# Optimization experiments

Measured on AMD Instinct MI355X. Metric: run time of the kernel, lower is better.

## Reference

```python
import jax, jax.numpy as jnp
import numpy as np

B, S, D, N, L, V = 4, 2048, 512, 16, 4, 256
EPS = 1e-5


def layernorm(x, g, b):
    m = x.mean(-1, keepdims=True)
    v = ((x - m) ** 2).mean(-1, keepdims=True)
    return (x - m) * jax.lax.rsqrt(v + EPS) * g + b


def ssm_layer(x, logA, Wd, bd, WB, bB, WC, bC, WDp, bDp, g, be):
    # x: (B,S,D)
    h = layernorm(x, g, be)
    delta = jax.nn.softplus(h @ Wd + bd)          # (B,S,D)
    Bi = h @ WB + bB                              # (B,S,N)
    Ci = h @ WC + bC                              # (B,S,N)
    A = -jnp.exp(logA)                            # (D,N)

    def step(state, inp):
        d_t, b_t, c_t, h_t = inp                  # (B,D),(B,N),(B,N),(B,D)
        dA = jnp.exp(d_t[:, :, None] * A)         # (B,D,N)
        state = dA * state + (d_t * h_t)[:, :, None] * b_t[:, None, :]
        y_t = jnp.einsum('bdn,bn->bd', state, c_t)
        return state, y_t

    xs = (jnp.moveaxis(delta, 1, 0), jnp.moveaxis(Bi, 1, 0),
          jnp.moveaxis(Ci, 1, 0), jnp.moveaxis(h, 1, 0))
    init = jnp.zeros((x.shape[0], x.shape[2], logA.shape[-1]), x.dtype)
    _, ys = jax.lax.scan(step, init, xs)
    y = jnp.moveaxis(ys, 0, 1)                    # (B,S,D)
    return x + y + h @ WDp + bDp


def setup_inputs() -> dict:
    key = jax.random.key(0)
    ks = jax.random.split(key, 12)
    s = 0.02
    byte_ids = jax.random.randint(ks[0], (B, S), 0, 256)
    emb_byte = jax.random.normal(ks[1], (V, D), jnp.float32) * s
    emb_pos = jax.random.normal(ks[2], (S, D), jnp.float32) * s
    logA = jnp.tile(jnp.log(jnp.linspace(1.0, N, N, dtype=jnp.float32)), (L, D, 1))
    Wd = jax.random.normal(ks[3], (L, D, D), jnp.float32) * s
    bd = jnp.zeros((L, D), jnp.float32)
    WB = jax.random.normal(ks[4], (L, D, N), jnp.float32) * s
    bB = jnp.zeros((L, N), jnp.float32)
    WC = jax.random.normal(ks[5], (L, D, N), jnp.float32) * s
    bC = jnp.zeros((L, N), jnp.float32)
    WDp = jax.random.normal(ks[6], (L, D, D), jnp.float32) * s
    bDp = jnp.zeros((L, D), jnp.float32)
    gamma = jnp.ones((L, D), jnp.float32)
    beta = jnp.zeros((L, D), jnp.float32)
    Wh = jax.random.normal(ks[7], (D, V), jnp.float32) * s
    bh = jnp.zeros((V,), jnp.float32)
    return {'byte_ids': byte_ids, 'emb_byte': emb_byte, 'emb_pos': emb_pos,
            'logA': logA, 'Wd': Wd, 'bd': bd, 'WB': WB, 'bB': bB,
            'WC': WC, 'bC': bC, 'WDp': WDp, 'bDp': bDp,
            'gamma': gamma, 'beta': beta, 'Wh': Wh, 'bh': bh}


def reference(byte_ids, emb_byte, emb_pos, logA, Wd, bd, WB, bB, WC, bC,
              WDp, bDp, gamma, beta, Wh, bh):
    S_ = byte_ids.shape[1]
    h = emb_byte[byte_ids] + emb_pos[:S_]
    for l in range(Wd.shape[0]):
        h = ssm_layer(h, logA[l], Wd[l], bd[l], WB[l], bB[l], WC[l], bC[l],
                      WDp[l], bDp[l], gamma[l], beta[l])
    return h @ Wh + bh                            # (B,S,256) logits
```

## Files before the change

### kernel.cpp

```cpp
#include <hip/hip_runtime.h>
#include <math.h>

#define BB 4
#define SS 2048
#define DD 512
#define NN 16
#define LL 4
#define VV 256
#define CC 64
#define TT (SS / CC)
#define EPSL 1e-5f
#define MM (BB * SS)
#define KI 16
#define LPAD 528

typedef __bf16 bf16;
typedef __attribute__((ext_vector_type(8))) __bf16 bf16x8;
typedef __attribute__((ext_vector_type(4))) __bf16 bf16x4;
typedef __attribute__((ext_vector_type(4))) float f32x4;


#define GLD_LDS(g, l) \
    __builtin_amdgcn_global_load_lds((__attribute__((address_space(1))) void*)(void*)(g), \
                                     (__attribute__((address_space(3))) void*)(l), 16, 0, 0)

__device__ __forceinline__ void ln_row_write(float4 v0, float4 v1, int lane, size_t row,
                                             const float* __restrict__ gamma,
                                             const float* __restrict__ beta,
                                             float* HN, bf16* HNb) {
    float s = v0.x + v0.y + v0.z + v0.w + v1.x + v1.y + v1.z + v1.w;
    float q = v0.x * v0.x + v0.y * v0.y + v0.z * v0.z + v0.w * v0.w +
              v1.x * v1.x + v1.y * v1.y + v1.z * v1.z + v1.w * v1.w;
#pragma unroll
    for (int o = 1; o < 64; o <<= 1) {
        s += __shfl_xor(s, o);
        q += __shfl_xor(q, o);
    }
    float m = s * (1.0f / DD);
    float var = q * (1.0f / DD) - m * m;
    float rs = rsqrtf(var + EPSL);
    float4 g0 = *(const float4*)(gamma + lane * 4);
    float4 g1 = *(const float4*)(gamma + 256 + lane * 4);
    float4 b0 = *(const float4*)(beta + lane * 4);
    float4 b1 = *(const float4*)(beta + 256 + lane * 4);
    float4 o0, o1;
    o0.x = (v0.x - m) * rs * g0.x + b0.x;
    o0.y = (v0.y - m) * rs * g0.y + b0.y;
    o0.z = (v0.z - m) * rs * g0.z + b0.z;
    o0.w = (v0.w - m) * rs * g0.w + b0.w;
    o1.x = (v1.x - m) * rs * g1.x + b1.x;
    o1.y = (v1.y - m) * rs * g1.y + b1.y;
    o1.z = (v1.z - m) * rs * g1.z + b1.z;
    o1.w = (v1.w - m) * rs * g1.w + b1.w;
    float* hr = HN + row * DD;
    *(float4*)(hr + lane * 4) = o0;
    *(float4*)(hr + 256 + lane * 4) = o1;
    size_t pb = (size_t)(row >> 4) * 8192 + (size_t)(lane >> 3) * 512 +
                (size_t)((lane & 7) >> 1) * 128 + (row & 15) * 8 + (lane & 1) * 4;
    bf16x4 p0 = {(bf16)o0.x, (bf16)o0.y, (bf16)o0.z, (bf16)o0.w};
    bf16x4 p1 = {(bf16)o1.x, (bf16)o1.y, (bf16)o1.z, (bf16)o1.w};
    *(bf16x4*)(HNb + pb) = p0;
    *(bf16x4*)(HNb + pb + 8 * 512) = p1;
}

__global__ void embed_ln(const int* __restrict__ ids,
                         const float* __restrict__ eb,
                         const float* __restrict__ ep,
                         const float* __restrict__ gamma,
                         const float* __restrict__ beta,
                         float* __restrict__ X, float* HN, bf16* HNb) {
    int wave = threadIdx.x >> 6;
    int lane = threadIdx.x & 63;
    size_t row = blockIdx.x * 4 + wave;
    int s = (int)(row & (SS - 1));
    int id = ids[row];
    const float* ebr = eb + (size_t)id * DD;
    const float* epr = ep + (size_t)s * DD;
    float4 e0 = *(const float4*)(ebr + lane * 4);
    float4 e1 = *(const float4*)(ebr + 256 + lane * 4);
    float4 p0 = *(const float4*)(epr + lane * 4);
    float4 p1 = *(const float4*)(epr + 256 + lane * 4);
    float4 v0 = {e0.x + p0.x, e0.y + p0.y, e0.z + p0.z, e0.w + p0.w};
    float4 v1 = {e1.x + p1.x, e1.y + p1.y, e1.z + p1.z, e1.w + p1.w};
    *(float4*)(X + row * DD + lane * 4) = v0;
    *(float4*)(X + row * DD + 256 + lane * 4) = v1;
    ln_row_write(v0, v1, lane, row, gamma, beta, HN, HNb);
}

__global__ __launch_bounds__(256) void convert_weights(const float* __restrict__ Wd,
                                                       const float* __restrict__ WDp,
                                                       const float* __restrict__ Wh,
                                                       bf16* __restrict__ WtP) {
    __shared__ float slab[512 * 17];
    int blk = blockIdx.x;
    const float* src;
    int nsrc, col0;
    bf16* dst;
    if (blk < 256) {
        int l = blk >> 6, tile = blk & 63;
        src = (tile < 32) ? (Wd + (size_t)l * DD * DD) : (WDp + (size_t)l * DD * DD);
        col0 = (tile & 31) * 16;
        nsrc = DD;
        dst = WtP + ((size_t)l * 64 + tile) * 8192;
    } else {
        int tile = blk - 256;
        src = Wh;
        col0 = tile * 16;
        nsrc = VV;
        dst = WtP + (size_t)(256 + tile) * 8192;
    }
    int tid = threadIdx.x;
    int kr = tid >> 2, cq = tid & 3;
#pragma unroll
    for (int i = 0; i < 8; i++) {
        int k = i * 64 + kr;
        float4 v = *(const float4*)(src + (size_t)k * nsrc + col0 + cq * 4);
        slab[k * 17 + cq * 4 + 0] = v.x;
        slab[k * 17 + cq * 4 + 1] = v.y;
        slab[k * 17 + cq * 4 + 2] = v.z;
        slab[k * 17 + cq * 4 + 3] = v.w;
    }
    __syncthreads();
#pragma unroll
    for (int it = 0; it < 4; it++) {
        int c = it * 256 + tid;
        int ki = c >> 6, fq = (c >> 4) & 3, fm = c & 15;
        int k0 = ki * 32 + fq * 8;
        bf16x8 v;
#pragma unroll
        for (int e = 0; e < 8; e++) v[e] = (bf16)slab[(k0 + e) * 17 + fm];
        *(bf16x8*)(dst + (size_t)c * 8) = v;
    }
}

template <int MODE, int NT>
__global__ __launch_bounds__(256, 8) void gemm_pack(const bf16* __restrict__ Ap,
                                                    const bf16* __restrict__ Bp,
                                                    const float* __restrict__ bias,
                                                    const float* __restrict__ bias2,
                                                    const float* __restrict__ Xres,
                                                    float* __restrict__ O1,
                                                    float* __restrict__ O2, int Nout) {
    __shared__ bf16 As[4 * 512];
    __shared__ bf16 Bs[4 * 512];
    const int tid = threadIdx.x, wave = tid >> 6, lane = tid & 63;
    const int lin = blockIdx.x;
    const int xcd = lin & 7, i4 = lin >> 3;
    const int ms = xcd * 16 + (i4 & 15);
    const int nb = i4 >> 4;

    const bf16* gA = Ap + ((size_t)ms * 4 + wave) * 8192 + lane * 8;
    const bf16* gB = Bp + ((size_t)nb * 4 + wave) * 8192 + lane * 8;
    bf16* lA = As + wave * 512;
    bf16* lB = Bs + wave * 512;

    const int fa0 = (wave >> 1) * 2, fb0 = (wave & 1) * 2;

    f32x4 acc[2][2];
#pragma unroll
    for (int i = 0; i < 2; i++)
#pragma unroll
        for (int j = 0; j < 2; j++) acc[i][j] = (f32x4){0.f, 0.f, 0.f, 0.f};

    for (int ki = 0; ki < KI; ki++) {
        GLD_LDS(gA + ki * 512, lA);
        GLD_LDS(gB + ki * 512, lB);
        __syncthreads();
        bf16x8 af[2], bfr[2];
#pragma unroll
        for (int i = 0; i < 2; i++) af[i] = *(const bf16x8*)(As + (fa0 + i) * 512 + lane * 8);
#pragma unroll
        for (int j = 0; j < 2; j++) bfr[j] = *(const bf16x8*)(Bs + (fb0 + j) * 512 + lane * 8);
#pragma unroll
        for (int i = 0; i < 2; i++)
#pragma unroll
            for (int j = 0; j < 2; j++)
                acc[i][j] = __builtin_amdgcn_mfma_f32_16x16x32_bf16(af[i], bfr[j], acc[i][j], 0, 0, 0);
        __syncthreads();
    }

    const int fm = lane & 15, fq = lane >> 4;
#pragma unroll
    for (int i = 0; i < 2; i++) {
#pragma unroll
        for (int j = 0; j < 2; j++) {
            int col = (nb * 4 + fb0 + j) * 16 + fm;
#pragma unroll
            for (int r = 0; r < 4; r++) {
                int row = (ms * 4 + fa0 + i) * 16 + fq * 4 + r;
                float v = acc[i][j][r];
                if (MODE == 0) {
                    O1[(size_t)row * Nout + col] = v + bias[col];
                } else {
                    if (col < DD) {
                        v += bias[col];
                        v = fmaxf(v, 0.0f) + log1pf(__expf(-fabsf(v)));
                        O1[(size_t)row * DD + col] = v;
                    } else {
                        int c = col - DD;
                        O2[(size_t)row * DD + c] = v + bias2[c] + Xres[(size_t)row * DD + c];
                    }
                }
            }
        }
    }
}

__global__ void gemmBC(const float* __restrict__ HN,
                       const float* __restrict__ WB, const float* __restrict__ bB,
                       const float* __restrict__ WC, const float* __restrict__ bC,
                       float* __restrict__ BI, float* __restrict__ CI) {
    int tid = threadIdx.x;
    int col = tid & 15;
    int row = blockIdx.x * 16 + (tid >> 4);
    const float* ar = HN + (size_t)row * DD;
    float accB = 0.0f, accC = 0.0f;
#pragma unroll 8
    for (int k = 0; k < DD; k++) {
        float a = ar[k];
        accB = fmaf(a, WB[k * NN + col], accB);
        accC = fmaf(a, WC[k * NN + col], accC);
    }
    BI[(size_t)row * NN + col] = accB + bB[col];
    CI[(size_t)row * NN + col] = accC + bC[col];
}

__global__ __launch_bounds__(512) void scan1(const float* __restrict__ DEL,
                                             const float* __restrict__ HN,
                                             const float* __restrict__ BI,
                                             const float* __restrict__ logA,
                                             float* __restrict__ P,
                                             float* __restrict__ LSt) {
    int b = blockIdx.x / CC, c = blockIdx.x % CC;
    int d = threadIdx.x;
    float Ar[NN], prod[NN], st[NN];
#pragma unroll
    for (int n = 0; n < NN; n++) {
        Ar[n] = -__expf(logA[d * NN + n]);
        prod[n] = 1.0f;
        st[n] = 0.0f;
    }
    size_t row0 = (size_t)b * SS + c * TT;
    for (int tt = 0; tt < TT; tt++) {
        size_t base = row0 + tt;
        float dl = DEL[base * DD + d];
        float du = dl * HN[base * DD + d];
        const float* bi = BI + base * NN;
#pragma unroll
        for (int n = 0; n < NN; n++) {
            float a = __expf(dl * Ar[n]);
            prod[n] *= a;
            st[n] = fmaf(a, st[n], du * bi[n]);
        }
    }
    size_t o = (((size_t)b * DD + d) * CC + c) * NN;
#pragma unroll
    for (int n = 0; n < NN; n++) {
        P[o + n] = prod[n];
        LSt[o + n] = st[n];
    }
}

__global__ void scan2(const float* __restrict__ P, float* __restrict__ LS) {
    int tid = blockIdx.x * 256 + threadIdx.x;
    int n = tid & (NN - 1);
    int d = (tid / NN) & (DD - 1);
    int b = tid / (NN * DD);
    size_t base = ((size_t)b * DD + d) * CC;
    float s = 0.0f;
    for (int c = 0; c < CC; c++) {
        size_t o = base * NN + (size_t)c * NN + n;
        float p = P[o];
        float ls = LS[o];
        LS[o] = s;
        s = fmaf(p, s, ls);
    }
}

template <int LAST>
__global__ __launch_bounds__(512) void scan3ln(const float* __restrict__ DEL,
                                               float* HN,
                                               const float* __restrict__ BI,
                                               const float* __restrict__ CI,
                                               const float* __restrict__ logA,
                                               const float* __restrict__ SIN,
                                               const float* __restrict__ D2,
                                               const float* __restrict__ gamma,
                                               const float* __restrict__ beta,
                                               float* __restrict__ X,
                                               bf16* HNb) {
    __shared__ float xvs[32 * LPAD];
    int b = blockIdx.x / CC, c = blockIdx.x % CC;
    int d = threadIdx.x;
    float Ar[NN], st[NN];
    size_t o = (((size_t)b * DD + d) * CC + c) * NN;
#pragma unroll
    for (int n = 0; n < NN; n++) {
        Ar[n] = -__expf(logA[d * NN + n]);
        st[n] = SIN[o + n];
    }
    size_t row0 = (size_t)b * SS + c * TT;
    for (int tt = 0; tt < TT; tt++) {
        size_t base = row0 + tt;
        float dl = DEL[base * DD + d];
        float du = dl * HN[base * DD + d];
        const float* bi = BI + base * NN;
        const float* ci = CI + base * NN;
        float y = 0.0f;
#pragma unroll
        for (int n = 0; n < NN; n++) {
            float a = __expf(dl * Ar[n]);
            st[n] = fmaf(a, st[n], du * bi[n]);
            y = fmaf(st[n], ci[n], y);
        }
        float xv = D2[base * DD + d] + y;
        xvs[tt * LPAD + d] = xv;
        if (!LAST) X[base * DD + d] = xv;
    }
    __syncthreads();
    int wv = d >> 6, lane = d & 63;
#pragma unroll
    for (int r = 0; r < 4; r++) {
        int tt = wv * 4 + r;
        size_t row = row0 + tt;
        const float* xr = xvs + tt * LPAD;
        float4 v0 = *(const float4*)(xr + lane * 4);
        float4 v1 = *(const float4*)(xr + 256 + lane * 4);
        if (LAST) {
            size_t pb = (size_t)(row >> 4) * 8192 + (size_t)(lane >> 3) * 512 +
                        (size_t)((lane & 7) >> 1) * 128 + (row & 15) * 8 + (lane & 1) * 4;
            bf16x4 p0 = {(bf16)v0.x, (bf16)v0.y, (bf16)v0.z, (bf16)v0.w};
            bf16x4 p1 = {(bf16)v1.x, (bf16)v1.y, (bf16)v1.z, (bf16)v1.w};
            *(bf16x4*)(HNb + pb) = p0;
            *(bf16x4*)(HNb + pb + 8 * 512) = p1;
        } else {
            ln_row_write(v0, v1, lane, row, gamma, beta, HN, HNb);
        }
    }
}

extern "C" void kernel_launch(void* const* d_in, const int* in_sizes, int n_in,
                              void* d_out, int out_size, void* d_ws, size_t ws_size,
                              hipStream_t stream) {
    const int* ids = (const int*)d_in[0];
    const float* eb = (const float*)d_in[1];
    const float* ep = (const float*)d_in[2];
    const float* logA = (const float*)d_in[3];
    const float* Wd = (const float*)d_in[4];
    const float* bd = (const float*)d_in[5];
    const float* WB = (const float*)d_in[6];
    const float* bB = (const float*)d_in[7];
    const float* WC = (const float*)d_in[8];
    const float* bC = (const float*)d_in[9];
    const float* WDp = (const float*)d_in[10];
    const float* bDp = (const float*)d_in[11];
    const float* gamma = (const float*)d_in[12];
    const float* beta = (const float*)d_in[13];
    const float* Wh = (const float*)d_in[14];
    const float* bh = (const float*)d_in[15];
    float* out = (float*)d_out;

    size_t E = (size_t)MM * DD;
    size_t EN = (size_t)MM * NN;
    size_t EC = (size_t)BB * DD * CC * NN;
    float* X = (float*)d_ws;
    float* HN = X + E;
    float* DEL = HN + E;
    float* D2 = DEL + E;
    float* BIc = D2 + E;
    float* CIc = BIc + EN;
    float* P = CIc + EN;
    float* LS = P + EC;
    bf16* HNb = (bf16*)(LS + EC);
    bf16* WtP = HNb + E;

    embed_ln<<<MM / 4, 256, 0, stream>>>(ids, eb, ep, gamma, beta, X, HN, HNb);
    convert_weights<<<272, 256, 0, stream>>>(Wd, WDp, Wh, WtP);
    for (int l = 0; l < LL; l++) {
        const float* lA = logA + (size_t)l * DD * NN;
        gemm_pack<1, 16><<<2048, 256, 0, stream>>>(
            HNb, WtP + (size_t)l * 524288, bd + l * DD, bDp + l * DD, X, DEL, D2, 1024);
        gemmBC<<<MM / 16, 256, 0, stream>>>(HN, WB + (size_t)l * DD * NN, bB + l * NN,
                                            WC + (size_t)l * DD * NN, bC + l * NN, BIc, CIc);
        scan1<<<BB * CC, 512, 0, stream>>>(DEL, HN, BIc, lA, P, LS);
        scan2<<<(BB * DD * NN) / 256, 256, 0, stream>>>(P, LS);
        if (l < LL - 1) {
            scan3ln<0><<<BB * CC, 512, 0, stream>>>(DEL, HN, BIc, CIc, lA, LS, D2,
                                                    gamma + (l + 1) * DD, beta + (l + 1) * DD,
                                                    X, HNb);
        } else {
            scan3ln<1><<<BB * CC, 512, 0, stream>>>(DEL, HN, BIc, CIc, lA, LS, D2,
                                                    nullptr, nullptr, X, HNb);
        }
    }
    gemm_pack<0, 4><<<512, 256, 0, stream>>>(
        HNb, WtP + (size_t)2097152, bh, nullptr, nullptr, out, nullptr, VV);
}
```

Baseline: 546.7 us.

## Fuse B/C projection and three-pass chunked scan into one cooperative kernel

Replaces the gemmBC, scan1, scan2 and scan3ln launches with a single cooperative kernel that uses grid.sync between phases. Each block computes its chunk's B/C projections into shared memory and keeps delta and delta*h in registers across the first and third passes instead of re-reading them from global memory. The layernorm is now done with wave shuffles and no longer stages the chunk through a large shared buffer. This removes launch overhead and intermediate BI/CI traffic, at the cost of higher register pressure (arrays of 32 elements per thread), two grid-wide barriers, and a middle scan pass that runs on only 64 blocks.

```diff
diff --git a/kernel.cpp b/kernel.cpp
--- a/kernel.cpp
+++ b/kernel.cpp
@@ -1,4 +1,5 @@
 #include <hip/hip_runtime.h>
+#include <hip/hip_cooperative_groups.h>
 #include <math.h>
 
 #define BB 4
@@ -12,7 +13,8 @@
 #define EPSL 1e-5f
 #define MM (BB * SS)
 #define KI 16
-#define LPAD 528
+
+namespace cg = cooperative_groups;
 
 typedef __bf16 bf16;
 typedef __attribute__((ext_vector_type(8))) __bf16 bf16x8;
@@ -206,136 +208,142 @@
     }
 }
 
-__global__ void gemmBC(const float* __restrict__ HN,
-                       const float* __restrict__ WB, const float* __restrict__ bB,
-                       const float* __restrict__ WC, const float* __restrict__ bC,
-                       float* __restrict__ BI, float* __restrict__ CI) {
-    int tid = threadIdx.x;
-    int col = tid & 15;
-    int row = blockIdx.x * 16 + (tid >> 4);
-    const float* ar = HN + (size_t)row * DD;
-    float accB = 0.0f, accC = 0.0f;
+template <int LAST>
+__global__ __launch_bounds__(512, 2) void scan_coop(
+        const float* __restrict__ DEL, float* HN,
+        const float* __restrict__ WB, const float* __restrict__ bB,
+        const float* __restrict__ WC, const float* __restrict__ bC,
+        const float* __restrict__ logA, const float* __restrict__ D2,
+        const float* __restrict__ gamma, const float* __restrict__ beta,
+        float* __restrict__ X, bf16* __restrict__ HNb,
+        float* __restrict__ P, float* __restrict__ LS) {
+    cg::grid_group grid = cg::this_grid();
+    __shared__ float bis[TT * NN];
+    __shared__ float cis[TT * NN];
+    __shared__ float wred[2][8][TT];
+    __shared__ float rstat[TT * 2];
+
+    const int lin = blockIdx.x;
+    const int b = lin / CC, c = lin % CC;
+    const int tid = threadIdx.x;
+    const size_t row0 = (size_t)b * SS + c * TT;
+
+    {
+        int row = tid >> 4, col = tid & 15;
+        const float* hr = HN + (row0 + row) * DD;
+        float aB = 0.0f, aC = 0.0f;
 #pragma unroll 8
-    for (int k = 0; k < DD; k++) {
-        float a = ar[k];
-        accB = fmaf(a, WB[k * NN + col], accB);
-        accC = fmaf(a, WC[k * NN + col], accC);
-    }
-    BI[(size_t)row * NN + col] = accB + bB[col];
-    CI[(size_t)row * NN + col] = accC + bC[col];
-}
-
-__global__ __launch_bounds__(512) void scan1(const float* __restrict__ DEL,
-                                             const float* __restrict__ HN,
-                                             const float* __restrict__ BI,
-                                             const float* __restrict__ logA,
-                                             float* __restrict__ P,
-                                             float* __restrict__ LSt) {
-    int b = blockIdx.x / CC, c = blockIdx.x % CC;
-    int d = threadIdx.x;
-    float Ar[NN], prod[NN], st[NN];
+        for (int k = 0; k < DD; k++) {
+            float h = hr[k];
+            aB = fmaf(h, WB[k * NN + col], aB);
+            aC = fmaf(h, WC[k * NN + col], aC);
+        }
+        bis[row * NN + col] = aB + bB[col];
+        cis[row * NN + col] = aC + bC[col];
+    }
+    __syncthreads();
+
+    const int d = tid;
+    float Ar[NN], st[NN], prod[NN], dl[TT], du[TT];
 #pragma unroll
     for (int n = 0; n < NN; n++) {
         Ar[n] = -__expf(logA[d * NN + n]);
         prod[n] = 1.0f;
         st[n] = 0.0f;
     }
-    size_t row0 = (size_t)b * SS + c * TT;
+#pragma unroll
     for (int tt = 0; tt < TT; tt++) {
         size_t base = row0 + tt;
-        float dl = DEL[base * DD + d];
-        float du = dl * HN[base * DD + d];
-        const float* bi = BI + base * NN;
+        dl[tt] = DEL[base * DD + d];
+        du[tt] = dl[tt] * HN[base * DD + d];
 #pragma unroll
         for (int n = 0; n < NN; n++) {
-            float a = __expf(dl * Ar[n]);
+            float a = __expf(dl[tt] * Ar[n]);
             prod[n] *= a;
-            st[n] = fmaf(a, st[n], du * bi[n]);
-        }
-    }
-    size_t o = (((size_t)b * DD + d) * CC + c) * NN;
+            st[n] = fmaf(a, st[n], du[tt] * bis[tt * NN + n]);
+        }
+    }
+    const size_t o = (((size_t)b * DD + d) * CC + c) * NN;
 #pragma unroll
     for (int n = 0; n < NN; n++) {
         P[o + n] = prod[n];
-        LSt[o + n] = st[n];
-    }
-}
-
-__global__ void scan2(const float* __restrict__ P, float* __restrict__ LS) {
-    int tid = blockIdx.x * 256 + threadIdx.x;
-    int n = tid & (NN - 1);
-    int d = (tid / NN) & (DD - 1);
-    int b = tid / (NN * DD);
-    size_t base = ((size_t)b * DD + d) * CC;
-    float s = 0.0f;
-    for (int c = 0; c < CC; c++) {
-        size_t o = base * NN + (size_t)c * NN + n;
-        float p = P[o];
-        float ls = LS[o];
-        LS[o] = s;
-        s = fmaf(p, s, ls);
-    }
-}
-
-template <int LAST>
-__global__ __launch_bounds__(512) void scan3ln(const float* __restrict__ DEL,
-                                               float* HN,
-                                               const float* __restrict__ BI,
-                                               const float* __restrict__ CI,
-                                               const float* __restrict__ logA,
-                                               const float* __restrict__ SIN,
-                                               const float* __restrict__ D2,
-                                               const float* __restrict__ gamma,
-                                               const float* __restrict__ beta,
-                                               float* __restrict__ X,
-                                               bf16* HNb) {
-    __shared__ float xvs[32 * LPAD];
-    int b = blockIdx.x / CC, c = blockIdx.x % CC;
-    int d = threadIdx.x;
-    float Ar[NN], st[NN];
-    size_t o = (((size_t)b * DD + d) * CC + c) * NN;
-#pragma unroll
-    for (int n = 0; n < NN; n++) {
-        Ar[n] = -__expf(logA[d * NN + n]);
-        st[n] = SIN[o + n];
-    }
-    size_t row0 = (size_t)b * SS + c * TT;
+        LS[o + n] = st[n];
+    }
+    grid.sync();
+
+    if (lin < 64) {
+        int g = lin * 512 + tid;
+        int n2 = g & (NN - 1);
+        int d2 = (g >> 4) & (DD - 1);
+        int b2 = g >> 13;
+        size_t base2 = ((size_t)b2 * DD + d2) * CC;
+        float s = 0.0f;
+        for (int c2 = 0; c2 < CC; c2++) {
+            size_t oo = (base2 + c2) * NN + n2;
+            float p = P[oo];
+            float ls = LS[oo];
+            LS[oo] = s;
+            s = fmaf(p, s, ls);
+        }
+    }
+    grid.sync();
+
+    float xv[TT];
+#pragma unroll
+    for (int n = 0; n < NN; n++) st[n] = LS[o + n];
+#pragma unroll
     for (int tt = 0; tt < TT; tt++) {
         size_t base = row0 + tt;
-        float dl = DEL[base * DD + d];
-        float du = dl * HN[base * DD + d];
-        const float* bi = BI + base * NN;
-        const float* ci = CI + base * NN;
         float y = 0.0f;
 #pragma unroll
         for (int n = 0; n < NN; n++) {
-            float a = __expf(dl * Ar[n]);
-            st[n] = fmaf(a, st[n], du * bi[n]);
-            y = fmaf(st[n], ci[n], y);
-        }
-        float xv = D2[base * DD + d] + y;
-        xvs[tt * LPAD + d] = xv;
-        if (!LAST) X[base * DD + d] = xv;
-    }
-    __syncthreads();
-    int wv = d >> 6, lane = d & 63;
-#pragma unroll
-    for (int r = 0; r < 4; r++) {
-        int tt = wv * 4 + r;
+            float a = __expf(dl[tt] * Ar[n]);
+            st[n] = fmaf(a, st[n], du[tt] * bis[tt * NN + n]);
+            y = fmaf(st[n], cis[tt * NN + n], y);
+        }
+        xv[tt] = D2[base * DD + d] + y;
+        if (!LAST) X[base * DD + d] = xv[tt];
+    }
+
+    const int wv = tid >> 6, lane = tid & 63;
+    if (!LAST) {
+#pragma unroll
+        for (int tt = 0; tt < TT; tt++) {
+            float s1 = xv[tt], s2 = xv[tt] * xv[tt];
+#pragma unroll
+            for (int ofs = 1; ofs < 64; ofs <<= 1) {
+                s1 += __shfl_xor(s1, ofs);
+                s2 += __shfl_xor(s2, ofs);
+            }
+            if (lane == 0) { wred[0][wv][tt] = s1; wred[1][wv][tt] = s2; }
+        }
+        __syncthreads();
+        if (tid < TT) {
+            float s1 = 0.0f, s2 = 0.0f;
+#pragma unroll
+            for (int w = 0; w < 8; w++) { s1 += wred[0][w][tid]; s2 += wred[1][w][tid]; }
+            float m = s1 * (1.0f / DD);
+            float var = s2 * (1.0f / DD) - m * m;
+            rstat[tid * 2] = m;
+            rstat[tid * 2 + 1] = rsqrtf(var + EPSL);
+        }
+        __syncthreads();
+    }
+
+    float gd = 1.0f, bd_ = 0.0f;
+    if (!LAST) { gd = gamma[d]; bd_ = beta[d]; }
+    const int ki2 = d >> 5, fq2 = (d >> 3) & 3, e2 = d & 7;
+#pragma unroll
+    for (int tt = 0; tt < TT; tt++) {
         size_t row = row0 + tt;
-        const float* xr = xvs + tt * LPAD;
-        float4 v0 = *(const float4*)(xr + lane * 4);
-        float4 v1 = *(const float4*)(xr + 256 + lane * 4);
+        float ov;
         if (LAST) {
-            size_t pb = (size_t)(row >> 4) * 8192 + (size_t)(lane >> 3) * 512 +
-                        (size_t)((lane & 7) >> 1) * 128 + (row & 15) * 8 + (lane & 1) * 4;
-            bf16x4 p0 = {(bf16)v0.x, (bf16)v0.y, (bf16)v0.z, (bf16)v0.w};
-            bf16x4 p1 = {(bf16)v1.x, (bf16)v1.y, (bf16)v1.z, (bf16)v1.w};
-            *(bf16x4*)(HNb + pb) = p0;
-            *(bf16x4*)(HNb + pb + 8 * 512) = p1;
+            ov = xv[tt];
         } else {
-            ln_row_write(v0, v1, lane, row, gamma, beta, HN, HNb);
-        }
+            ov = (xv[tt] - rstat[tt * 2]) * rstat[tt * 2 + 1] * gd + bd_;
+            HN[row * DD + d] = ov;
+        }
+        HNb[(size_t)(row >> 4) * 8192 + ki2 * 512 + fq2 * 128 + (row & 15) * 8 + e2] = (bf16)ov;
     }
 }
 
@@ -361,15 +369,12 @@
     float* out = (float*)d_out;
 
     size_t E = (size_t)MM * DD;
-    size_t EN = (size_t)MM * NN;
     size_t EC = (size_t)BB * DD * CC * NN;
     float* X = (float*)d_ws;
     float* HN = X + E;
     float* DEL = HN + E;
     float* D2 = DEL + E;
-    float* BIc = D2 + E;
-    float* CIc = BIc + EN;
-    float* P = CIc + EN;
+    float* P = D2 + E;
     float* LS = P + EC;
     bf16* HNb = (bf16*)(LS + EC);
     bf16* WtP = HNb + E;
@@ -380,17 +385,22 @@
         const float* lA = logA + (size_t)l * DD * NN;
         gemm_pack<1, 16><<<2048, 256, 0, stream>>>(
             HNb, WtP + (size_t)l * 524288, bd + l * DD, bDp + l * DD, X, DEL, D2, 1024);
-        gemmBC<<<MM / 16, 256, 0, stream>>>(HN, WB + (size_t)l * DD * NN, bB + l * NN,
-                                            WC + (size_t)l * DD * NN, bC + l * NN, BIc, CIc);
-        scan1<<<BB * CC, 512, 0, stream>>>(DEL, HN, BIc, lA, P, LS);
-        scan2<<<(BB * DD * NN) / 256, 256, 0, stream>>>(P, LS);
+        const float* lWB = WB + (size_t)l * DD * NN;
+        const float* lbB = bB + (size_t)l * NN;
+        const float* lWC = WC + (size_t)l * DD * NN;
+        const float* lbC = bC + (size_t)l * NN;
+        const float* lg = gamma + (size_t)((l + 1 < LL) ? (l + 1) : l) * DD;
+        const float* lbe = beta + (size_t)((l + 1 < LL) ? (l + 1) : l) * DD;
+        void* args[] = {(void*)&DEL, (void*)&HN, (void*)&lWB, (void*)&lbB,
+                        (void*)&lWC, (void*)&lbC, (void*)&lA, (void*)&D2,
+                        (void*)&lg, (void*)&lbe, (void*)&X, (void*)&HNb,
+                        (void*)&P, (void*)&LS};
         if (l < LL - 1) {
-            scan3ln<0><<<BB * CC, 512, 0, stream>>>(DEL, HN, BIc, CIc, lA, LS, D2,
-                                                    gamma + (l + 1) * DD, beta + (l + 1) * DD,
-                                                    X, HNb);
+            hipLaunchCooperativeKernel((void*)scan_coop<0>, dim3(BB * CC), dim3(512),
+                                       args, 0, stream);
         } else {
-            scan3ln<1><<<BB * CC, 512, 0, stream>>>(DEL, HN, BIc, CIc, lA, LS, D2,
-                                                    nullptr, nullptr, X, HNb);
+            hipLaunchCooperativeKernel((void*)scan_coop<1>, dim3(BB * CC), dim3(512),
+                                       args, 0, stream);
         }
     }
     gemm_pack<0, 4><<<512, 256, 0, stream>>>(
```

New measurement: 1.451 ms. 2.65x slower.

## Replace fp32 normalized activations with per-row LN stats and fuse small kernels

Applied to the files above, without the earlier changes.

Stops writing the fp32 layernorm output. Each row instead stores its mean and rsqrt pair, and scan1, scan3 and the B/C projection recompute the normalized value from X, gamma and beta. The B/C projection runs as extra blocks inside the main GEMM launch, and the embedding and weight-conversion kernels are merged into one launch. This removes a large buffer write and its repeated reads each layer, plus a few launches, at the cost of some extra per-element arithmetic and a mixed-role GEMM grid.

```diff
diff --git a/kernel.cpp b/kernel.cpp
--- a/kernel.cpp
+++ b/kernel.cpp
@@ -24,10 +24,11 @@
     __builtin_amdgcn_global_load_lds((__attribute__((address_space(1))) void*)(void*)(g), \
                                      (__attribute__((address_space(3))) void*)(l), 16, 0, 0)
 
-__device__ __forceinline__ void ln_row_write(float4 v0, float4 v1, int lane, size_t row,
-                                             const float* __restrict__ gamma,
-                                             const float* __restrict__ beta,
-                                             float* HN, bf16* HNb) {
+__device__ __forceinline__ void ln_row_pack(float4 v0, float4 v1, int lane, size_t row,
+                                            const float* __restrict__ gamma,
+                                            const float* __restrict__ beta,
+                                            float2* __restrict__ stats,
+                                            bf16* __restrict__ HNb) {
     float s = v0.x + v0.y + v0.z + v0.w + v1.x + v1.y + v1.z + v1.w;
     float q = v0.x * v0.x + v0.y * v0.y + v0.z * v0.z + v0.w * v0.w +
               v1.x * v1.x + v1.y * v1.y + v1.z * v1.z + v1.w * v1.w;
@@ -39,6 +40,7 @@
     float m = s * (1.0f / DD);
     float var = q * (1.0f / DD) - m * m;
     float rs = rsqrtf(var + EPSL);
+    if (lane == 0) stats[row] = make_float2(m, rs);
     float4 g0 = *(const float4*)(gamma + lane * 4);
     float4 g1 = *(const float4*)(gamma + 256 + lane * 4);
     float4 b0 = *(const float4*)(beta + lane * 4);
@@ -52,9 +54,6 @@
     o1.y = (v1.y - m) * rs * g1.y + b1.y;
     o1.z = (v1.z - m) * rs * g1.z + b1.z;
     o1.w = (v1.w - m) * rs * g1.w + b1.w;
-    float* hr = HN + row * DD;
-    *(float4*)(hr + lane * 4) = o0;
-    *(float4*)(hr + 256 + lane * 4) = o1;
     size_t pb = (size_t)(row >> 4) * 8192 + (size_t)(lane >> 3) * 512 +
                 (size_t)((lane & 7) >> 1) * 128 + (row & 15) * 8 + (lane & 1) * 4;
     bf16x4 p0 = {(bf16)o0.x, (bf16)o0.y, (bf16)o0.z, (bf16)o0.w};
@@ -63,36 +62,39 @@
     *(bf16x4*)(HNb + pb + 8 * 512) = p1;
 }
 
-__global__ void embed_ln(const int* __restrict__ ids,
-                         const float* __restrict__ eb,
-                         const float* __restrict__ ep,
-                         const float* __restrict__ gamma,
-                         const float* __restrict__ beta,
-                         float* __restrict__ X, float* HN, bf16* HNb) {
-    int wave = threadIdx.x >> 6;
-    int lane = threadIdx.x & 63;
-    size_t row = blockIdx.x * 4 + wave;
-    int s = (int)(row & (SS - 1));
-    int id = ids[row];
-    const float* ebr = eb + (size_t)id * DD;
-    const float* epr = ep + (size_t)s * DD;
-    float4 e0 = *(const float4*)(ebr + lane * 4);
-    float4 e1 = *(const float4*)(ebr + 256 + lane * 4);
-    float4 p0 = *(const float4*)(epr + lane * 4);
-    float4 p1 = *(const float4*)(epr + 256 + lane * 4);
-    float4 v0 = {e0.x + p0.x, e0.y + p0.y, e0.z + p0.z, e0.w + p0.w};
-    float4 v1 = {e1.x + p1.x, e1.y + p1.y, e1.z + p1.z, e1.w + p1.w};
-    *(float4*)(X + row * DD + lane * 4) = v0;
-    *(float4*)(X + row * DD + 256 + lane * 4) = v1;
-    ln_row_write(v0, v1, lane, row, gamma, beta, HN, HNb);
-}
-
-__global__ __launch_bounds__(256) void convert_weights(const float* __restrict__ Wd,
-                                                       const float* __restrict__ WDp,
-                                                       const float* __restrict__ Wh,
-                                                       bf16* __restrict__ WtP) {
+__global__ __launch_bounds__(256) void embed_conv(const int* __restrict__ ids,
+                                                  const float* __restrict__ eb,
+                                                  const float* __restrict__ ep,
+                                                  const float* __restrict__ gamma,
+                                                  const float* __restrict__ beta,
+                                                  const float* __restrict__ Wd,
+                                                  const float* __restrict__ WDp,
+                                                  const float* __restrict__ Wh,
+                                                  float* __restrict__ X,
+                                                  float2* __restrict__ stats,
+                                                  bf16* __restrict__ HNb,
+                                                  bf16* __restrict__ WtP) {
     __shared__ float slab[512 * 17];
-    int blk = blockIdx.x;
+    if (blockIdx.x < 2048) {
+        int wave = threadIdx.x >> 6;
+        int lane = threadIdx.x & 63;
+        size_t row = blockIdx.x * 4 + wave;
+        int s = (int)(row & (SS - 1));
+        int id = ids[row];
+        const float* ebr = eb + (size_t)id * DD;
+        const float* epr = ep + (size_t)s * DD;
+        float4 e0 = *(const float4*)(ebr + lane * 4);
+        float4 e1 = *(const float4*)(ebr + 256 + lane * 4);
+        float4 p0 = *(const float4*)(epr + lane * 4);
+        float4 p1 = *(const float4*)(epr + 256 + lane * 4);
+        float4 v0 = {e0.x + p0.x, e0.y + p0.y, e0.z + p0.z, e0.w + p0.w};
+        float4 v1 = {e1.x + p1.x, e1.y + p1.y, e1.z + p1.z, e1.w + p1.w};
+        *(float4*)(X + row * DD + lane * 4) = v0;
+        *(float4*)(X + row * DD + 256 + lane * 4) = v1;
+        ln_row_pack(v0, v1, lane, row, gamma, beta, stats, HNb);
+        return;
+    }
+    int blk = blockIdx.x - 2048;
     const float* src;
     int nsrc, col0;
     bf16* dst;
@@ -133,18 +135,45 @@
     }
 }
 
-template <int MODE, int NT>
+template <int MODE, int NT, int BC>
 __global__ __launch_bounds__(256, 8) void gemm_pack(const bf16* __restrict__ Ap,
                                                     const bf16* __restrict__ Bp,
                                                     const float* __restrict__ bias,
                                                     const float* __restrict__ bias2,
                                                     const float* __restrict__ Xres,
+                                                    const float2* __restrict__ stats,
+                                                    const float* __restrict__ gamma,
+                                                    const float* __restrict__ beta,
+                                                    const float* __restrict__ WB,
+                                                    const float* __restrict__ bB,
+                                                    const float* __restrict__ WC,
+                                                    const float* __restrict__ bC,
                                                     float* __restrict__ O1,
-                                                    float* __restrict__ O2, int Nout) {
+                                                    float* __restrict__ O2,
+                                                    float* __restrict__ BI,
+                                                    float* __restrict__ CI, int Nout) {
     __shared__ bf16 As[4 * 512];
     __shared__ bf16 Bs[4 * 512];
-    const int tid = threadIdx.x, wave = tid >> 6, lane = tid & 63;
     const int lin = blockIdx.x;
+    const int tid = threadIdx.x;
+    if (BC && lin >= 128 * NT) {
+        int blk = lin - 128 * NT;
+        int col = tid & 15;
+        int row = blk * 16 + (tid >> 4);
+        const float* xr = Xres + (size_t)row * DD;
+        float2 s2 = stats[row];
+        float accB = 0.0f, accC = 0.0f;
+#pragma unroll 8
+        for (int k = 0; k < DD; k++) {
+            float hn = (xr[k] - s2.x) * s2.y * gamma[k] + beta[k];
+            accB = fmaf(hn, WB[k * NN + col], accB);
+            accC = fmaf(hn, WC[k * NN + col], accC);
+        }
+        BI[(size_t)row * NN + col] = accB + bB[col];
+        CI[(size_t)row * NN + col] = accC + bC[col];
+        return;
+    }
+    const int wave = tid >> 6, lane = tid & 63;
     const int xcd = lin & 7, i4 = lin >> 3;
     const int ms = xcd * 16 + (i4 & 15);
     const int nb = i4 >> 4;
@@ -206,33 +235,18 @@
     }
 }
 
-__global__ void gemmBC(const float* __restrict__ HN,
-                       const float* __restrict__ WB, const float* __restrict__ bB,
-                       const float* __restrict__ WC, const float* __restrict__ bC,
-                       float* __restrict__ BI, float* __restrict__ CI) {
-    int tid = threadIdx.x;
-    int col = tid & 15;
-    int row = blockIdx.x * 16 + (tid >> 4);
-    const float* ar = HN + (size_t)row * DD;
-    float accB = 0.0f, accC = 0.0f;
-#pragma unroll 8
-    for (int k = 0; k < DD; k++) {
-        float a = ar[k];
-        accB = fmaf(a, WB[k * NN + col], accB);
-        accC = fmaf(a, WC[k * NN + col], accC);
-    }
-    BI[(size_t)row * NN + col] = accB + bB[col];
-    CI[(size_t)row * NN + col] = accC + bC[col];
-}
-
 __global__ __launch_bounds__(512) void scan1(const float* __restrict__ DEL,
-                                             const float* __restrict__ HN,
+                                             const float* __restrict__ X,
+                                             const float2* __restrict__ stats,
+                                             const float* __restrict__ gamma,
+                                             const float* __restrict__ beta,
                                              const float* __restrict__ BI,
                                              const float* __restrict__ logA,
                                              float* __restrict__ P,
                                              float* __restrict__ LSt) {
     int b = blockIdx.x / CC, c = blockIdx.x % CC;
     int d = threadIdx.x;
+    float gd = gamma[d], bd = beta[d];
     float Ar[NN], prod[NN], st[NN];
 #pragma unroll
     for (int n = 0; n < NN; n++) {
@@ -243,8 +257,10 @@
     size_t row0 = (size_t)b * SS + c * TT;
     for (int tt = 0; tt < TT; tt++) {
         size_t base = row0 + tt;
+        float2 s2 = stats[base];
         float dl = DEL[base * DD + d];
-        float du = dl * HN[base * DD + d];
+        float hn = (X[base * DD + d] - s2.x) * s2.y * gd + bd;
+        float du = dl * hn;
         const float* bi = BI + base * NN;
 #pragma unroll
         for (int n = 0; n < NN; n++) {
@@ -279,19 +295,22 @@
 
 template <int LAST>
 __global__ __launch_bounds__(512) void scan3ln(const float* __restrict__ DEL,
-                                               float* HN,
+                                               float* __restrict__ X,
+                                               float2* __restrict__ stats,
+                                               const float* __restrict__ gcur,
+                                               const float* __restrict__ bcur,
                                                const float* __restrict__ BI,
                                                const float* __restrict__ CI,
                                                const float* __restrict__ logA,
                                                const float* __restrict__ SIN,
                                                const float* __restrict__ D2,
-                                               const float* __restrict__ gamma,
-                                               const float* __restrict__ beta,
-                                               float* __restrict__ X,
-                                               bf16* HNb) {
+                                               const float* __restrict__ gnext,
+                                               const float* __restrict__ bnext,
+                                               bf16* __restrict__ HNb) {
     __shared__ float xvs[32 * LPAD];
     int b = blockIdx.x / CC, c = blockIdx.x % CC;
     int d = threadIdx.x;
+    float gd = gcur[d], bd = bcur[d];
     float Ar[NN], st[NN];
     size_t o = (((size_t)b * DD + d) * CC + c) * NN;
 #pragma unroll
@@ -302,8 +321,11 @@
     size_t row0 = (size_t)b * SS + c * TT;
     for (int tt = 0; tt < TT; tt++) {
         size_t base = row0 + tt;
+        float2 s2 = stats[base];
         float dl = DEL[base * DD + d];
-        float du = dl * HN[base * DD + d];
+        float x = X[base * DD + d];
+        float hn = (x - s2.x) * s2.y * gd + bd;
+        float du = dl * hn;
         const float* bi = BI + base * NN;
         const float* ci = CI + base * NN;
         float y = 0.0f;
@@ -334,7 +356,7 @@
             *(bf16x4*)(HNb + pb) = p0;
             *(bf16x4*)(HNb + pb + 8 * 512) = p1;
         } else {
-            ln_row_write(v0, v1, lane, row, gamma, beta, HN, HNb);
+            ln_row_pack(v0, v1, lane, row, gnext, bnext, stats, HNb);
         }
     }
 }
@@ -364,35 +386,41 @@
     size_t EN = (size_t)MM * NN;
     size_t EC = (size_t)BB * DD * CC * NN;
     float* X = (float*)d_ws;
-    float* HN = X + E;
-    float* DEL = HN + E;
+    float* DEL = X + E;
     float* D2 = DEL + E;
-    float* BIc = D2 + E;
+    float* P = D2 + E;
+    float* LS = P + EC;
+    float* BIc = LS + EC;
     float* CIc = BIc + EN;
-    float* P = CIc + EN;
-    float* LS = P + EC;
-    bf16* HNb = (bf16*)(LS + EC);
+    float2* stats = (float2*)(CIc + EN);
+    bf16* HNb = (bf16*)(stats + MM);
     bf16* WtP = HNb + E;
 
-    embed_ln<<<MM / 4, 256, 0, stream>>>(ids, eb, ep, gamma, beta, X, HN, HNb);
-    convert_weights<<<272, 256, 0, stream>>>(Wd, WDp, Wh, WtP);
+    embed_conv<<<2048 + 272, 256, 0, stream>>>(ids, eb, ep, gamma, beta,
+                                               Wd, WDp, Wh, X, stats, HNb, WtP);
     for (int l = 0; l < LL; l++) {
         const float* lA = logA + (size_t)l * DD * NN;
-        gemm_pack<1, 16><<<2048, 256, 0, stream>>>(
-            HNb, WtP + (size_t)l * 524288, bd + l * DD, bDp + l * DD, X, DEL, D2, 1024);
-        gemmBC<<<MM / 16, 256, 0, stream>>>(HN, WB + (size_t)l * DD * NN, bB + l * NN,
-                                            WC + (size_t)l * DD * NN, bC + l * NN, BIc, CIc);
-        scan1<<<BB * CC, 512, 0, stream>>>(DEL, HN, BIc, lA, P, LS);
+        const float* lg = gamma + (size_t)l * DD;
+        const float* lb = beta + (size_t)l * DD;
+        gemm_pack<1, 16, 1><<<2048 + 512, 256, 0, stream>>>(
+            HNb, WtP + (size_t)l * 524288, bd + l * DD, bDp + l * DD, X,
+            stats, lg, lb,
+            WB + (size_t)l * DD * NN, bB + l * NN,
+            WC + (size_t)l * DD * NN, bC + l * NN,
+            DEL, D2, BIc, CIc, 1024);
+        scan1<<<BB * CC, 512, 0, stream>>>(DEL, X, stats, lg, lb, BIc, lA, P, LS);
         scan2<<<(BB * DD * NN) / 256, 256, 0, stream>>>(P, LS);
         if (l < LL - 1) {
-            scan3ln<0><<<BB * CC, 512, 0, stream>>>(DEL, HN, BIc, CIc, lA, LS, D2,
-                                                    gamma + (l + 1) * DD, beta + (l + 1) * DD,
-                                                    X, HNb);
+            scan3ln<0><<<BB * CC, 512, 0, stream>>>(DEL, X, stats, lg, lb, BIc, CIc,
+                                                    lA, LS, D2,
+                                                    gamma + (size_t)(l + 1) * DD,
+                                                    beta + (size_t)(l + 1) * DD, HNb);
         } else {
-            scan3ln<1><<<BB * CC, 512, 0, stream>>>(DEL, HN, BIc, CIc, lA, LS, D2,
-                                                    nullptr, nullptr, X, HNb);
-        }
-    }
-    gemm_pack<0, 4><<<512, 256, 0, stream>>>(
-        HNb, WtP + (size_t)2097152, bh, nullptr, nullptr, out, nullptr, VV);
-}
+            scan3ln<1><<<BB * CC, 512, 0, stream>>>(DEL, X, stats, lg, lb, BIc, CIc,
+                                                    lA, LS, D2, lg, lb, HNb);
+        }
+    }
+    gemm_pack<0, 4, 0><<<512, 256, 0, stream>>>(
+        HNb, WtP + (size_t)2097152, bh, nullptr, nullptr, nullptr, nullptr, nullptr,
+        nullptr, nullptr, nullptr, nullptr, out, nullptr, nullptr, nullptr, VV);
+}
```

After: 585.9 us. +7.2%, slower.
